# Performance work log

Measured on AMD Instinct MI355X. Metric: run time of the kernel, lower is better.

The kernel has to match this reference:

```python
import jax, jax.numpy as jnp
import numpy as np
from jax import lax

B, C, H, W, P = 16, 256, 64, 64, 4
EPS = 1e-5


def setup_inputs() -> dict:
    key = jax.random.key(0)
    ks = jax.random.split(key, 16)
    s = 0.05
    d = {
        'rgb': jax.random.normal(ks[0], (B, C, H, W), jnp.float32),
        'th': jax.random.normal(ks[1], (B, C, H, W), jnp.float32),
        'q_w': jax.random.normal(ks[2], (C, C), jnp.float32) * s,
        'q_b': jax.random.normal(ks[3], (C,), jnp.float32) * s,
        'kvr_w': jax.random.normal(ks[4], (2 * C, C), jnp.float32) * s,
        'kvr_b': jax.random.normal(ks[5], (2 * C,), jnp.float32) * s,
        'kvt_w': jax.random.normal(ks[6], (2 * C, C), jnp.float32) * s,
        'kvt_b': jax.random.normal(ks[7], (2 * C,), jnp.float32) * s,
        'offr_w': jax.random.normal(ks[8], (2 * P, C, 3, 3), jnp.float32) * s,
        'offr_b': jax.random.normal(ks[9], (2 * P,), jnp.float32) * s,
        'offt_w': jax.random.normal(ks[10], (2 * P, C, 3, 3), jnp.float32) * s,
        'offt_b': jax.random.normal(ks[11], (2 * P,), jnp.float32) * s,
        'out_w': jax.random.normal(ks[12], (C, 2 * C), jnp.float32) * s,
        'out_b': jax.random.normal(ks[13], (C,), jnp.float32) * s,
        'gamma': jnp.ones((C,), jnp.float32),
        'beta': jnp.zeros((C,), jnp.float32),
    }
    return d


def conv1x1(x, w, b):
    # x: [B,Ci,H,W], w: [Co,Ci] -> [B,Co,H,W]
    return jnp.einsum('bchw,oc->bohw', x, w) + b[None, :, None, None]


def conv3x3(x, w, b):
    y = lax.conv_general_dilated(x, w, (1, 1), 'SAME',
                                 dimension_numbers=('NCHW', 'OIHW', 'NCHW'))
    return y + b[None, :, None, None]


def deform_sample(feat, offset):
    # feat: [B,C,H,W]; offset: [B,2P,H,W] (pixel-unit offsets, (x,y) pairs)
    Bs, Cs, Hs, Ws = feat.shape
    off = offset.reshape(Bs, -1, 2, Hs, Ws)  # [B,P,2,H,W]
    # base grid in [-1,1], align_corners=True convention
    gy = jnp.linspace(-1.0, 1.0, Hs)[None, None, :, None]
    gx = jnp.linspace(-1.0, 1.0, Ws)[None, None, None, :]
    grid_x = gx + off[:, :, 0] / (Ws / 2.0)  # [B,P,H,W]
    grid_y = gy + off[:, :, 1] / (Hs / 2.0)
    # normalized -> pixel coords (align_corners=True)
    x = (grid_x + 1.0) * (Ws - 1) / 2.0
    y = (grid_y + 1.0) * (Hs - 1) / 2.0
    x0 = jnp.floor(x)
    y0 = jnp.floor(y)
    wx = x - x0
    wy = y - y0
    feat_flat = feat.reshape(Bs, Cs, Hs * Ws)

    def corner(xi, yi, wgt):
        valid = (xi >= 0) & (xi < Ws) & (yi >= 0) & (yi < Hs)  # zeros padding
        xc = jnp.clip(xi, 0, Ws - 1).astype(jnp.int32)
        yc = jnp.clip(yi, 0, Hs - 1).astype(jnp.int32)
        idx = (yc * Ws + xc).reshape(Bs, 1, -1)  # [B,1,P*H*W]
        g = jnp.take_along_axis(feat_flat, jnp.broadcast_to(idx, (Bs, Cs, idx.shape[-1])), axis=2)
        g = g.reshape(Bs, Cs, -1, Hs, Ws)  # [B,C,P,H,W]
        w_eff = (wgt * valid.astype(feat.dtype))[:, None]  # [B,1,P,H,W]
        return g * w_eff

    x0i = x0.astype(jnp.int32)
    y0i = y0.astype(jnp.int32)
    out = (corner(x0i, y0i, (1 - wx) * (1 - wy))
           + corner(x0i + 1, y0i, wx * (1 - wy))
           + corner(x0i, y0i + 1, (1 - wx) * wy)
           + corner(x0i + 1, y0i + 1, wx * wy))
    return out.mean(axis=2)  # mean over P -> [B,C,H,W]


def batchnorm_train(x, gamma, beta):
    mu = x.mean(axis=(0, 2, 3), keepdims=True)
    var = x.var(axis=(0, 2, 3), keepdims=True)
    xn = (x - mu) * lax.rsqrt(var + EPS)
    return xn * gamma[None, :, None, None] + beta[None, :, None, None]


def reference(rgb, th, q_w, q_b, kvr_w, kvr_b, kvt_w, kvt_b,
              offr_w, offr_b, offt_w, offt_b, out_w, out_b, gamma, beta):
    q_rgb = conv1x1(rgb, q_w, q_b)
    q_th = conv1x1(th, q_w, q_b)
    kv_rgb = conv1x1(rgb, kvr_w, kvr_b)
    kv_th = conv1x1(th, kvt_w, kvt_b)
    v_rgb = kv_rgb[:, C:]  # k_rgb = kv_rgb[:, :C] is unused downstream
    v_th = kv_th[:, C:]
    off_rgb2th = conv3x3(th, offr_w, offr_b)
    off_th2rgb = conv3x3(rgb, offt_w, offt_b)
    v_rgb2th = deform_sample(v_rgb, off_rgb2th)
    v_th2rgb = deform_sample(v_th, off_th2rgb)
    attn_rgb = jax.nn.sigmoid(q_rgb) * v_th2rgb
    attn_th = jax.nn.sigmoid(q_th) * v_rgb2th
    fused = conv1x1(jnp.concatenate([attn_rgb, attn_th], axis=1), out_w, out_b)
    return batchnorm_train(fused + 0.5 * (rgb + th), gamma, beta)
```

## Files before the change

kernel.cpp:

```cpp
#include <hip/hip_runtime.h>

typedef __bf16 bf16x8 __attribute__((ext_vector_type(8)));
typedef float  f32x4  __attribute__((ext_vector_type(4)));

constexpr int Bn = 16, Cn = 256, Hn = 64, Wn = 64, HWn = 64 * 64;
constexpr int Ntot = Bn * HWn;

#define DEV static __device__ __forceinline__

DEV unsigned short f2bf(float f) {
  unsigned u = __builtin_bit_cast(unsigned, f);
  u += 0x7fffu + ((u >> 16) & 1u);
  return (unsigned short)(u >> 16);
}
DEV float bf2f(unsigned short s) {
  unsigned u = ((unsigned)s) << 16;
  return __builtin_bit_cast(float, u);
}
DEV bf16x8 asbf(uint4 u) { return __builtin_bit_cast(bf16x8, u); }

__global__ void k_prep(const float* qw, const float* kvrw, const float* kvtw,
                       const float* offrw, const float* offtw, const float* outw,
                       unsigned short* Aqv, unsigned short* Aoff, unsigned short* Aout) {
  int idx = blockIdx.x * 256 + threadIdx.x;
  if (idx < 2 * 512 * 256) {
    int t = idx >> 17; int r = idx & 131071; int o = r >> 8; int c = r & 255;
    float v = (o < 256) ? qw[o * 256 + c] : (t ? kvtw[o * 256 + c] : kvrw[o * 256 + c]);
    Aqv[idx] = f2bf(v);
    return;
  }
  idx -= 2 * 512 * 256;
  if (idx < 2 * 16 * 2304) {
    int t = idx / 36864; int r = idx % 36864;
    int o = r / 2304; int rc = r % 2304; int tap = rc >> 8; int c = rc & 255;
    const float* w = t ? offtw : offrw;
    float v = (o < 8) ? w[(o * 256 + c) * 9 + tap] : 0.f;
    Aoff[idx] = f2bf(v);
    return;
  }
  idx -= 2 * 16 * 2304;
  if (idx < 256 * 512) Aout[idx] = f2bf(outw[idx]);
}

__global__ void k_transpose(const float* rgb, const float* th, unsigned short* xT) {
  int bi = blockIdx.x;
  int ct = bi & 3;
  int nt = (bi >> 2) & 63;
  int b  = (bi >> 8) & 15;
  int t  = bi >> 12;
  const float* src = t ? th : rgb;
  int c0 = ct * 64, n0 = nt * 64;
  __shared__ float tile[64][65];
  int tid = threadIdx.x;
  int nl = tid & 63, cg = tid >> 6;
#pragma unroll
  for (int i = 0; i < 16; i++) {
    int c = cg * 16 + i;
    tile[c][nl] = src[(size_t)(b * 256 + c0 + c) * HWn + n0 + nl];
  }
  __syncthreads();
  int pr = tid >> 2, sg = tid & 3;
  unsigned short tmp[16];
#pragma unroll
  for (int j = 0; j < 16; j++) tmp[j] = f2bf(tile[sg * 16 + j][pr]);
  unsigned short* dst = xT + (size_t)t * Ntot * 256 +
                        (size_t)(b * HWn + n0 + pr) * 256 + c0 + sg * 16;
  *(uint4*)(dst)     = *(const uint4*)(tmp);
  *(uint4*)(dst + 8) = *(const uint4*)(tmp + 8);
}

__global__ __launch_bounds__(512, 2) void k_qv(
    const unsigned short* Aqv, const unsigned short* xT,
    const float* qb, const float* kvrb, const float* kvtb,
    unsigned short* qs, unsigned short* vv) {
  __shared__ unsigned short smem[32768];
  int t  = blockIdx.z;
  int mt = blockIdx.y;
  int nt = blockIdx.x;
  int swznt = ((nt & 7) << 6) | (nt >> 3);
  int o0 = mt * 128;
  int n0 = swznt * 128;
  int tid = threadIdx.x;
  const unsigned short* Aq = Aqv + t * 512 * 256;
  const unsigned short* Xg = xT + (size_t)t * Ntot * 256 + (size_t)n0 * 256;

  auto stage = [&](int kb, int bb) {
    unsigned short* As = smem + bb * 8192;
    unsigned short* Xs = smem + 16384 + bb * 8192;
#pragma unroll
    for (int i = 0; i < 2; i++) {
      int cid = tid + i * 512;
      int row = cid >> 3, seg = cid & 7;
      int ss = seg ^ (row & 7);
      *(uint4*)(&As[row * 64 + seg * 8]) =
          *(const uint4*)(Aq + (size_t)(o0 + row) * 256 + kb * 64 + ss * 8);
    }
#pragma unroll
    for (int i = 0; i < 2; i++) {
      int cid = tid + i * 512;
      int row = cid >> 3, seg = cid & 7;
      int ss = seg ^ (row & 7);
      *(uint4*)(&Xs[row * 64 + seg * 8]) =
          *(const uint4*)(Xg + (size_t)row * 256 + kb * 64 + ss * 8);
    }
  };

  int w = __builtin_amdgcn_readfirstlane(tid >> 6);
  int lane = tid & 63;
  int wo = w & 1, wn = w >> 1;
  int r16 = lane & 15, q4 = lane >> 4;

  f32x4 acc[4][2];
#pragma unroll
  for (int a = 0; a < 4; a++) { acc[a][0] = f32x4{0.f,0.f,0.f,0.f}; acc[a][1] = f32x4{0.f,0.f,0.f,0.f}; }

  stage(0, 0);
  __syncthreads();
#pragma unroll
  for (int kb = 0; kb < 4; kb++) {
    if (kb < 3) stage(kb + 1, (kb + 1) & 1);
    const unsigned short* As = smem + (kb & 1) * 8192;
    const unsigned short* Xs = smem + 16384 + (kb & 1) * 8192;
#pragma unroll
    for (int ks = 0; ks < 2; ks++) {
      uint4 af[4], bfr[2];
#pragma unroll
      for (int oi = 0; oi < 4; oi++) {
        int row = wo * 64 + oi * 16 + r16;
        int seg = (ks * 4 + q4) ^ (row & 7);
        af[oi] = *(const uint4*)(&As[row * 64 + seg * 8]);
      }
#pragma unroll
      for (int ni = 0; ni < 2; ni++) {
        int row = wn * 32 + ni * 16 + r16;
        int seg = (ks * 4 + q4) ^ (row & 7);
        bfr[ni] = *(const uint4*)(&Xs[row * 64 + seg * 8]);
      }
#pragma unroll
      for (int oi = 0; oi < 4; oi++)
#pragma unroll
        for (int ni = 0; ni < 2; ni++)
          acc[oi][ni] = __builtin_amdgcn_mfma_f32_16x16x32_bf16(
              asbf(af[oi]), asbf(bfr[ni]), acc[oi][ni], 0, 0, 0);
    }
    __syncthreads();
  }

  bool isq = (mt < 2);
  const float* bias = isq ? qb : (t ? kvtb : kvrb);
  float4 bv[4];
#pragma unroll
  for (int oi = 0; oi < 4; oi++)
    bv[oi] = *(const float4*)(&bias[o0 + wo * 64 + oi * 16 + q4 * 4]);
#pragma unroll
  for (int oi = 0; oi < 4; oi++) {
    int ol = wo * 64 + oi * 16 + q4 * 4;
#pragma unroll
    for (int ni = 0; ni < 2; ni++) {
      int nl = wn * 32 + ni * 16 + r16;
      unsigned short pk[4];
#pragma unroll
      for (int j = 0; j < 4; j++) {
        float val = acc[oi][ni][j] + ((const float*)&bv[oi])[j];
        if (isq) val = 1.f / (1.f + __expf(-val));
        pk[j] = f2bf(val);
      }
      *(uint2*)(&smem[nl * 132 + ol]) = *(const uint2*)(pk);
    }
  }
  __syncthreads();
  unsigned short* outp = (isq ? qs : vv) + (size_t)t * Ntot * 256 + (mt & 1) * 128;
#pragma unroll
  for (int pass = 0; pass < 4; pass++) {
    int nl = pass * 32 + (tid >> 4);
    int c  = tid & 15;
    uint4 vq = *(const uint4*)(&smem[nl * 132 + c * 8]);
    *(uint4*)(outp + (size_t)(n0 + nl) * 256 + c * 8) = vq;
  }
}

__global__ __launch_bounds__(256, 4) void k_off(
    const unsigned short* Aoff, const unsigned short* xT,
    const float* offrb, const float* offtb, float* offo) {
  __shared__ unsigned short Alds[9 * 8 * 264 + 264];
  int t  = blockIdx.y;
  int bh = blockIdx.x;
  int swz = ((bh & 7) << 7) | (bh >> 3);
  int b = swz >> 6, h = swz & 63;
  int tid = threadIdx.x;
  const unsigned short* Aw = Aoff + t * 36864;

#pragma unroll
  for (int i = 0; i < 9; i++) {
    int cid = tid + i * 256;
    int o = cid / 288;
    int rem = cid - o * 288;
    int tap = rem >> 5, cg = rem & 31;
    uint4 v = *(const uint4*)(Aw + o * 2304 + tap * 256 + cg * 8);
    *(uint4*)(&Alds[(tap * 8 + o) * 264 + cg * 8]) = v;
  }
  if (tid < 33) {
    uint4 z; z.x = 0; z.y = 0; z.z = 0; z.w = 0;
    *(uint4*)(&Alds[19008 + tid * 8]) = z;
  }
  __syncthreads();

  int lane = tid & 63, w = tid >> 6;
  int r16 = lane & 15, q4 = lane >> 4;
  int wl = w * 16 + r16;
  const unsigned short* xin = xT + (size_t)(t ? 0 : 1) * Ntot * 256;
  int zbase = 19008 + q4 * 8;
  int abase = r16 * 264 + q4 * 8;
  bool rowok = (r16 < 8);

  f32x4 acc = {0.f, 0.f, 0.f, 0.f};
  uint4 bufA[8], bufB[8];

#define LOADT(buf, tap) {                                                      \
    int dy = (tap) / 3 - 1, dx = (tap) % 3 - 1;                                \
    int hh = h + dy, ww = wl + dx;                                             \
    bool ok = (hh >= 0 && hh < 64 && ww >= 0 && ww < 64);                      \
    int hc = hh < 0 ? 0 : (hh > 63 ? 63 : hh);                                 \
    int wc = ww < 0 ? 0 : (ww > 63 ? 63 : ww);                                 \
    const unsigned short* p =                                                  \
        xin + (size_t)(((b * 64 + hc) * 64 + wc) * 256) + q4 * 8;              \
    _Pragma("unroll") for (int ks = 0; ks < 8; ks++) {                         \
      uint4 v = *(const uint4*)(p + ks * 32);                                  \
      if (!ok) { v.x = 0; v.y = 0; v.z = 0; v.w = 0; }                         \
      buf[ks] = v;                                                             \
    } }

#define COMPT(buf, tap) {                                                      \
    _Pragma("unroll") for (int ks = 0; ks < 8; ks++) {                         \
      int aofs = rowok ? ((tap) * 8 * 264 + abase + ks * 32) : (zbase + ks * 32); \
      uint4 af = *(const uint4*)(&Alds[aofs]);                                 \
      acc = __builtin_amdgcn_mfma_f32_16x16x32_bf16(asbf(af), asbf(buf[ks]),   \
                                                    acc, 0, 0, 0);             \
    } }

  LOADT(bufA, 0)
  LOADT(bufB, 1)
  COMPT(bufA, 0)
  LOADT(bufA, 2)
  COMPT(bufB, 1)
  LOADT(bufB, 3)
  COMPT(bufA, 2)
  LOADT(bufA, 4)
  COMPT(bufB, 3)
  LOADT(bufB, 5)
  COMPT(bufA, 4)
  LOADT(bufA, 6)
  COMPT(bufB, 5)
  LOADT(bufB, 7)
  COMPT(bufA, 6)
  LOADT(bufA, 8)
  COMPT(bufB, 7)
  COMPT(bufA, 8)
#undef LOADT
#undef COMPT

  if (lane < 32) {
    const float* ob = t ? offtb : offrb;
    int n = (b * 64 + h) * 64 + wl;
    float4 r;
    r.x = acc[0] + ob[q4 * 4 + 0];
    r.y = acc[1] + ob[q4 * 4 + 1];
    r.z = acc[2] + ob[q4 * 4 + 2];
    r.w = acc[3] + ob[q4 * 4 + 3];
    *(float4*)(offo + (size_t)t * Ntot * 8 + (size_t)n * 8 + q4 * 4) = r;
  }
}

__global__ void k_gather(const unsigned short* qs, const unsigned short* vv,
                         const float* offo, unsigned short* concat) {
  int tid = threadIdx.x;
  int bi  = blockIdx.x;
  int pass = blockIdx.y;
  int swz = ((bi & 7) << 9) | (bi >> 3);
  int chunk = tid & 15, pixL = tid >> 4;
  int n = swz * 16 + pixL;
  int b = n >> 12;
  int h = (n >> 6) & 63, pix = n & 63;
  const unsigned short* vsrc = vv + (size_t)(pass ? 0 : 1) * Ntot * 256;
  const float* offp          = offo + (size_t)(pass ? 0 : 1) * Ntot * 8;
  const unsigned short* qsrc = qs + (size_t)(pass ? 1 : 0) * Ntot * 256;
  float acc[16];
#pragma unroll
  for (int i = 0; i < 16; i++) acc[i] = 0.f;
#pragma unroll
  for (int p = 0; p < 4; p++) {
    float dx = offp[(size_t)n * 8 + 2 * p], dy = offp[(size_t)n * 8 + 2 * p + 1];
    float xf = (float)pix + dx * (63.f / 64.f);
    float yf = (float)h   + dy * (63.f / 64.f);
    float x0f = floorf(xf), y0f = floorf(yf);
    float wx = xf - x0f, wy = yf - y0f;
    int x0 = (int)x0f, y0 = (int)y0f;
#pragma unroll
    for (int cc = 0; cc < 4; cc++) {
      int cy = cc >> 1, cx = cc & 1;
      int ix = x0 + cx, iy = y0 + cy;
      bool ok = (ix >= 0 && ix < 64 && iy >= 0 && iy < 64);
      int ixc = ix < 0 ? 0 : (ix > 63 ? 63 : ix);
      int iyc = iy < 0 ? 0 : (iy > 63 ? 63 : iy);
      float wgt = (cx ? wx : 1.f - wx) * (cy ? wy : 1.f - wy);
      wgt = ok ? wgt : 0.f;
      const unsigned short* g =
          vsrc + (size_t)(((b * 64 + iyc) * 64 + ixc) * 256 + chunk * 16);
      uint4 raw0 = *(const uint4*)(g);
      uint4 raw1 = *(const uint4*)(g + 8);
      const unsigned short* r0 = (const unsigned short*)&raw0;
      const unsigned short* r1 = (const unsigned short*)&raw1;
#pragma unroll
      for (int e = 0; e < 8; e++) {
        acc[e]     += wgt * bf2f(r0[e]);
        acc[8 + e] += wgt * bf2f(r1[e]);
      }
    }
  }
  uint4 q0 = *(const uint4*)(qsrc + (size_t)n * 256 + chunk * 16);
  uint4 q1 = *(const uint4*)(qsrc + (size_t)n * 256 + chunk * 16 + 8);
  const unsigned short* qp0 = (const unsigned short*)&q0;
  const unsigned short* qp1 = (const unsigned short*)&q1;
  unsigned short pk[16];
#pragma unroll
  for (int e = 0; e < 8; e++) {
    pk[e]     = f2bf(0.25f * acc[e]     * bf2f(qp0[e]));
    pk[8 + e] = f2bf(0.25f * acc[8 + e] * bf2f(qp1[e]));
  }
  unsigned short* dst = concat + (size_t)n * 512 + pass * 256 + chunk * 16;
  *(uint4*)(dst)     = *(const uint4*)(pk);
  *(uint4*)(dst + 8) = *(const uint4*)(pk + 8);
}

__global__ __launch_bounds__(512, 2) void k_out(
    const unsigned short* Aout, const unsigned short* concat, const float* outb,
    const float* rgb, const float* th, float* dout, float* partial) {
  __shared__ unsigned short Asm[2][128 * 64];
  __shared__ unsigned short Xsm[2][128 * 64];
  __shared__ float bstat[128][2];
  int bi = blockIdx.x;
  int my = blockIdx.y;
  int swz = ((bi & 7) << 6) | (bi >> 3);
  int n0 = swz * 128;
  int o0 = my * 128;
  int tid = threadIdx.x;
  if (tid < 128) { bstat[tid][0] = 0.f; bstat[tid][1] = 0.f; }

  auto stage = [&](int kb, int bb) {
#pragma unroll
    for (int i = 0; i < 2; i++) {
      int cid = tid + i * 512;
      int row = cid >> 3, seg = cid & 7;
      int ss = seg ^ (row & 7);
      *(uint4*)(&Asm[bb][row * 64 + seg * 8]) =
          *(const uint4*)(Aout + (size_t)(o0 + row) * 512 + kb * 64 + ss * 8);
    }
#pragma unroll
    for (int i = 0; i < 2; i++) {
      int cid = tid + i * 512;
      int row = cid >> 3, seg = cid & 7;
      int ss = seg ^ (row & 7);
      *(uint4*)(&Xsm[bb][row * 64 + seg * 8]) =
          *(const uint4*)(concat + (size_t)(n0 + row) * 512 + kb * 64 + ss * 8);
    }
  };

  int w = __builtin_amdgcn_readfirstlane(tid >> 6);
  int lane = tid & 63;
  int wo = w & 1, wn = w >> 1;
  int r16 = lane & 15, q4 = lane >> 4;

  f32x4 acc2[4][2];
#pragma unroll
  for (int a = 0; a < 4; a++) { acc2[a][0] = f32x4{0.f,0.f,0.f,0.f}; acc2[a][1] = f32x4{0.f,0.f,0.f,0.f}; }

  stage(0, 0);
  __syncthreads();
#pragma unroll
  for (int kb = 0; kb < 8; kb++) {
    if (kb < 7) stage(kb + 1, (kb + 1) & 1);
    int bb = kb & 1;
#pragma unroll
    for (int ks = 0; ks < 2; ks++) {
      uint4 af[4], bfr[2];
#pragma unroll
      for (int oi = 0; oi < 4; oi++) {
        int row = wo * 64 + oi * 16 + r16;
        int seg = (ks * 4 + q4) ^ (row & 7);
        af[oi] = *(const uint4*)(&Asm[bb][row * 64 + seg * 8]);
      }
#pragma unroll
      for (int ni = 0; ni < 2; ni++) {
        int row = wn * 32 + ni * 16 + r16;
        int seg = (ks * 4 + q4) ^ (row & 7);
        bfr[ni] = *(const uint4*)(&Xsm[bb][row * 64 + seg * 8]);
      }
#pragma unroll
      for (int oi = 0; oi < 4; oi++)
#pragma unroll
        for (int ni = 0; ni < 2; ni++)
          acc2[oi][ni] = __builtin_amdgcn_mfma_f32_16x16x32_bf16(
              asbf(af[oi]), asbf(bfr[ni]), acc2[oi][ni], 0, 0, 0);
    }
    __syncthreads();
  }
#pragma unroll
  for (int oi = 0; oi < 4; oi++) {
    int obl = wo * 64 + oi * 16 + q4 * 4;
#pragma unroll
    for (int j = 0; j < 4; j++) {
      int ol = obl + j;
      int o = o0 + ol;
      float s1 = 0.f, s2 = 0.f;
#pragma unroll
      for (int ni = 0; ni < 2; ni++) {
        int pl = wn * 32 + ni * 16 + r16;
        int n = n0 + pl;
        int bI = n >> 12, hw = n & 4095;
        size_t gidx = (size_t)(bI * 256 + o) * HWn + hw;
        float val = acc2[oi][ni][j] + outb[o] + 0.5f * (rgb[gidx] + th[gidx]);
        dout[gidx] = val;
        s1 += val; s2 += val * val;
      }
#pragma unroll
      for (int m = 1; m < 16; m <<= 1) {
        s1 += __shfl_xor(s1, m, 16);
        s2 += __shfl_xor(s2, m, 16);
      }
      if (r16 == 0) { atomicAdd(&bstat[ol][0], s1); atomicAdd(&bstat[ol][1], s2); }
    }
  }
  __syncthreads();
  if (tid < 128) {
    partial[((size_t)my * 512 + bi) * 256 + tid]       = bstat[tid][0];
    partial[((size_t)my * 512 + bi) * 256 + 128 + tid] = bstat[tid][1];
  }
}

__global__ void k_stats(const float* partial, const float* gamma, const float* beta,
                        float* sstats) {
  int c = blockIdx.x, tid = threadIdx.x;
  int my = c >> 7, j = c & 127;
  float s1 = 0.f, s2 = 0.f;
  for (int i = tid; i < 512; i += 256) {
    const float* pp = partial + ((size_t)my * 512 + i) * 256;
    s1 += pp[j];
    s2 += pp[128 + j];
  }
  __shared__ float r1[256], r2[256];
  r1[tid] = s1; r2[tid] = s2;
  __syncthreads();
  for (int st = 128; st > 0; st >>= 1) {
    if (tid < st) { r1[tid] += r1[tid + st]; r2[tid] += r2[tid + st]; }
    __syncthreads();
  }
  if (tid == 0) {
    float mean = r1[0] / 65536.f;
    float var  = r2[0] / 65536.f - mean * mean;
    float scale = gamma[c] / sqrtf(var + 1e-5f);
    sstats[c]       = scale;
    sstats[256 + c] = beta[c] - mean * scale;
  }
}

__global__ void k_bn(float* dout, const float* sstats) {
  int idx = blockIdx.x * 256 + threadIdx.x;
  size_t base = (size_t)idx * 4;
  int c = (int)((base >> 12) & 255);
  float4 v = *(float4*)(dout + base);
  float sc = sstats[c], sh = sstats[256 + c];
  v.x = v.x * sc + sh; v.y = v.y * sc + sh;
  v.z = v.z * sc + sh; v.w = v.w * sc + sh;
  *(float4*)(dout + base) = v;
}

extern "C" void kernel_launch(void* const* d_in, const int* in_sizes, int n_in,
                              void* d_out, int out_size, void* d_ws, size_t ws_size,
                              hipStream_t stream) {
  const float* rgb   = (const float*)d_in[0];
  const float* th    = (const float*)d_in[1];
  const float* qw    = (const float*)d_in[2];
  const float* qb    = (const float*)d_in[3];
  const float* kvrw  = (const float*)d_in[4];
  const float* kvrb  = (const float*)d_in[5];
  const float* kvtw  = (const float*)d_in[6];
  const float* kvtb  = (const float*)d_in[7];
  const float* offrw = (const float*)d_in[8];
  const float* offrb = (const float*)d_in[9];
  const float* offtw = (const float*)d_in[10];
  const float* offtb = (const float*)d_in[11];
  const float* outw  = (const float*)d_in[12];
  const float* outb  = (const float*)d_in[13];
  const float* gamma = (const float*)d_in[14];
  const float* beta  = (const float*)d_in[15];
  float* dout = (float*)d_out;

  unsigned short* xT   = (unsigned short*)d_ws;
  unsigned short* qsb  = xT  + (size_t)2 * Ntot * 256;
  unsigned short* vvb  = qsb + (size_t)2 * Ntot * 256;
  float* offo          = (float*)(vvb + (size_t)2 * Ntot * 256);
  unsigned short* Aqv  = (unsigned short*)(offo + (size_t)2 * Ntot * 8);
  unsigned short* Aoff = Aqv + 2 * 512 * 256;
  unsigned short* Aout = Aoff + 2 * 16 * 2304;
  float* partial       = (float*)(Aout + 256 * 512);
  float* sstats        = partial + (size_t)1024 * 256;
  unsigned short* concat = xT;

  k_prep<<<1824, 256, 0, stream>>>(qw, kvrw, kvtw, offrw, offtw, outw, Aqv, Aoff, Aout);
  k_transpose<<<8192, 256, 0, stream>>>(rgb, th, xT);
  k_qv<<<dim3(512, 4, 2), 512, 0, stream>>>(Aqv, xT, qb, kvrb, kvtb, qsb, vvb);
  k_off<<<dim3(1024, 2), 256, 0, stream>>>(Aoff, xT, offrb, offtb, offo);
  k_gather<<<dim3(4096, 2), 256, 0, stream>>>(qsb, vvb, offo, concat);
  k_out<<<dim3(512, 2), 512, 0, stream>>>(Aout, concat, outb, rgb, th, dout, partial);
  k_stats<<<256, 256, 0, stream>>>(partial, gamma, beta, sstats);
  k_bn<<<16384, 256, 0, stream>>>(dout, sstats);
}
```

Before: 406.2 us.

## Fuse deformable gather into output projection GEMM via shared-memory concat tile

Merges the gather kernel and the output 1x1 conv GEMM into one kernel. Each block handles one image row of 64 pixels: it bilinearly samples and gates both streams into a 64x512 bf16 tile in LDS, then runs the 256-output MFMA GEMM straight from LDS with weight fragments read from global memory in a repacked layout. This removes the global concat write and reread and one launch. In exchange it uses 64 KB of LDS per block, loses the double-buffered staging of the weights, and doubles the number of BN partial rows.

Result: slower. 567.8 us (+39.8%).

```diff
diff --git a/kernel.cpp b/kernel.cpp
--- a/kernel.cpp
+++ b/kernel.cpp
@@ -39,7 +39,10 @@
     return;
   }
   idx -= 2 * 16 * 2304;
-  if (idx < 256 * 512) Aout[idx] = f2bf(outw[idx]);
+  if (idx < 256 * 512) {
+    int seg = idx >> 11, o = (idx >> 3) & 255, e = idx & 7;
+    Aout[idx] = f2bf(outw[o * 512 + seg * 8 + e]);
+  }
 }
 
 __global__ void k_transpose(const float* rgb, const float* th, unsigned short* xT) {
@@ -271,153 +274,122 @@
   }
 }
 
-__global__ void k_gather(const unsigned short* qs, const unsigned short* vv,
-                         const float* offo, unsigned short* concat) {
+__global__ __launch_bounds__(512, 2) void k_fuse(
+    const unsigned short* qs, const unsigned short* vv, const float* offo,
+    const unsigned short* Apk, const float* outb,
+    const float* rgb, const float* th, float* dout, float* partial) {
+  __shared__ unsigned short cc[64 * 512];
+  __shared__ float bstat[256][2];
   int tid = threadIdx.x;
   int bi  = blockIdx.x;
-  int pass = blockIdx.y;
-  int swz = ((bi & 7) << 9) | (bi >> 3);
-  int chunk = tid & 15, pixL = tid >> 4;
-  int n = swz * 16 + pixL;
-  int b = n >> 12;
-  int h = (n >> 6) & 63, pix = n & 63;
-  const unsigned short* vsrc = vv + (size_t)(pass ? 0 : 1) * Ntot * 256;
-  const float* offp          = offo + (size_t)(pass ? 0 : 1) * Ntot * 8;
-  const unsigned short* qsrc = qs + (size_t)(pass ? 1 : 0) * Ntot * 256;
-  float acc[16];
-#pragma unroll
-  for (int i = 0; i < 16; i++) acc[i] = 0.f;
-#pragma unroll
-  for (int p = 0; p < 4; p++) {
-    float dx = offp[(size_t)n * 8 + 2 * p], dy = offp[(size_t)n * 8 + 2 * p + 1];
-    float xf = (float)pix + dx * (63.f / 64.f);
-    float yf = (float)h   + dy * (63.f / 64.f);
-    float x0f = floorf(xf), y0f = floorf(yf);
-    float wx = xf - x0f, wy = yf - y0f;
-    int x0 = (int)x0f, y0 = (int)y0f;
-#pragma unroll
-    for (int cc = 0; cc < 4; cc++) {
-      int cy = cc >> 1, cx = cc & 1;
-      int ix = x0 + cx, iy = y0 + cy;
-      bool ok = (ix >= 0 && ix < 64 && iy >= 0 && iy < 64);
-      int ixc = ix < 0 ? 0 : (ix > 63 ? 63 : ix);
-      int iyc = iy < 0 ? 0 : (iy > 63 ? 63 : iy);
-      float wgt = (cx ? wx : 1.f - wx) * (cy ? wy : 1.f - wy);
-      wgt = ok ? wgt : 0.f;
-      const unsigned short* g =
-          vsrc + (size_t)(((b * 64 + iyc) * 64 + ixc) * 256 + chunk * 16);
-      uint4 raw0 = *(const uint4*)(g);
-      uint4 raw1 = *(const uint4*)(g + 8);
-      const unsigned short* r0 = (const unsigned short*)&raw0;
-      const unsigned short* r1 = (const unsigned short*)&raw1;
+  int swz = ((bi & 7) << 7) | (bi >> 3);
+  int b = swz >> 6, h = swz & 63;
+  if (tid < 256) { bstat[tid][0] = 0.f; bstat[tid][1] = 0.f; }
+
+  {
+    int px = tid >> 3, sub = tid & 7;
+    int pass = sub >> 2, qtr = sub & 3;
+    int n = (b * 64 + h) * 64 + px;
+    const unsigned short* vsrc = vv + (size_t)(pass ? 0 : 1) * Ntot * 256;
+    const float* offp          = offo + (size_t)(pass ? 0 : 1) * Ntot * 8 + (size_t)n * 8;
+    const unsigned short* qsrc = qs + (size_t)(pass ? 1 : 0) * Ntot * 256 + (size_t)n * 256;
+
+    int   coff[4][4];
+    float cwgt[4][4];
+#pragma unroll
+    for (int p = 0; p < 4; p++) {
+      float dx = offp[2 * p], dy = offp[2 * p + 1];
+      float xf = (float)px + dx * (63.f / 64.f);
+      float yf = (float)h  + dy * (63.f / 64.f);
+      float x0f = floorf(xf), y0f = floorf(yf);
+      float wx = xf - x0f, wy = yf - y0f;
+      int x0 = (int)x0f, y0 = (int)y0f;
+#pragma unroll
+      for (int c = 0; c < 4; c++) {
+        int cy2 = c >> 1, cx2 = c & 1;
+        int ix = x0 + cx2, iy = y0 + cy2;
+        bool ok = (ix >= 0 && ix < 64 && iy >= 0 && iy < 64);
+        int ixc = ix < 0 ? 0 : (ix > 63 ? 63 : ix);
+        int iyc = iy < 0 ? 0 : (iy > 63 ? 63 : iy);
+        coff[p][c] = ((b * 64 + iyc) * 64 + ixc) * 256;
+        float wgt = (cx2 ? wx : 1.f - wx) * (cy2 ? wy : 1.f - wy);
+        cwgt[p][c] = ok ? wgt : 0.f;
+      }
+    }
+#pragma unroll
+    for (int s = 0; s < 4; s++) {
+      int c0 = qtr * 64 + s * 16;
+      float acc[16];
+#pragma unroll
+      for (int i = 0; i < 16; i++) acc[i] = 0.f;
+#pragma unroll
+      for (int p = 0; p < 4; p++)
+#pragma unroll
+        for (int c = 0; c < 4; c++) {
+          const unsigned short* g = vsrc + coff[p][c] + c0;
+          float wgt = cwgt[p][c];
+          uint4 raw0 = *(const uint4*)(g);
+          uint4 raw1 = *(const uint4*)(g + 8);
+          const unsigned short* r0 = (const unsigned short*)&raw0;
+          const unsigned short* r1 = (const unsigned short*)&raw1;
+#pragma unroll
+          for (int e = 0; e < 8; e++) {
+            acc[e]     += wgt * bf2f(r0[e]);
+            acc[8 + e] += wgt * bf2f(r1[e]);
+          }
+        }
+      uint4 q0 = *(const uint4*)(qsrc + c0);
+      uint4 q1 = *(const uint4*)(qsrc + c0 + 8);
+      const unsigned short* qp0 = (const unsigned short*)&q0;
+      const unsigned short* qp1 = (const unsigned short*)&q1;
+      unsigned short pk[16];
 #pragma unroll
       for (int e = 0; e < 8; e++) {
-        acc[e]     += wgt * bf2f(r0[e]);
-        acc[8 + e] += wgt * bf2f(r1[e]);
-      }
-    }
-  }
-  uint4 q0 = *(const uint4*)(qsrc + (size_t)n * 256 + chunk * 16);
-  uint4 q1 = *(const uint4*)(qsrc + (size_t)n * 256 + chunk * 16 + 8);
-  const unsigned short* qp0 = (const unsigned short*)&q0;
-  const unsigned short* qp1 = (const unsigned short*)&q1;
-  unsigned short pk[16];
-#pragma unroll
-  for (int e = 0; e < 8; e++) {
-    pk[e]     = f2bf(0.25f * acc[e]     * bf2f(qp0[e]));
-    pk[8 + e] = f2bf(0.25f * acc[8 + e] * bf2f(qp1[e]));
-  }
-  unsigned short* dst = concat + (size_t)n * 512 + pass * 256 + chunk * 16;
-  *(uint4*)(dst)     = *(const uint4*)(pk);
-  *(uint4*)(dst + 8) = *(const uint4*)(pk + 8);
-}
-
-__global__ __launch_bounds__(512, 2) void k_out(
-    const unsigned short* Aout, const unsigned short* concat, const float* outb,
-    const float* rgb, const float* th, float* dout, float* partial) {
-  __shared__ unsigned short Asm[2][128 * 64];
-  __shared__ unsigned short Xsm[2][128 * 64];
-  __shared__ float bstat[128][2];
-  int bi = blockIdx.x;
-  int my = blockIdx.y;
-  int swz = ((bi & 7) << 6) | (bi >> 3);
-  int n0 = swz * 128;
-  int o0 = my * 128;
-  int tid = threadIdx.x;
-  if (tid < 128) { bstat[tid][0] = 0.f; bstat[tid][1] = 0.f; }
-
-  auto stage = [&](int kb, int bb) {
-#pragma unroll
-    for (int i = 0; i < 2; i++) {
-      int cid = tid + i * 512;
-      int row = cid >> 3, seg = cid & 7;
-      int ss = seg ^ (row & 7);
-      *(uint4*)(&Asm[bb][row * 64 + seg * 8]) =
-          *(const uint4*)(Aout + (size_t)(o0 + row) * 512 + kb * 64 + ss * 8);
-    }
-#pragma unroll
-    for (int i = 0; i < 2; i++) {
-      int cid = tid + i * 512;
-      int row = cid >> 3, seg = cid & 7;
-      int ss = seg ^ (row & 7);
-      *(uint4*)(&Xsm[bb][row * 64 + seg * 8]) =
-          *(const uint4*)(concat + (size_t)(n0 + row) * 512 + kb * 64 + ss * 8);
-    }
-  };
-
-  int w = __builtin_amdgcn_readfirstlane(tid >> 6);
-  int lane = tid & 63;
-  int wo = w & 1, wn = w >> 1;
+        pk[e]     = f2bf(0.25f * acc[e]     * bf2f(qp0[e]));
+        pk[8 + e] = f2bf(0.25f * acc[8 + e] * bf2f(qp1[e]));
+      }
+      int seg0 = pass * 32 + qtr * 8 + s * 2;
+      *(uint4*)(&cc[px * 512 + ((seg0    ) ^ (px & 7)) * 8]) = *(const uint4*)(pk);
+      *(uint4*)(&cc[px * 512 + ((seg0 + 1) ^ (px & 7)) * 8]) = *(const uint4*)(pk + 8);
+    }
+  }
+  __syncthreads();
+
+  int lane = tid & 63, wv = tid >> 6;
+  int wo = wv >> 1, wn = wv & 1;
   int r16 = lane & 15, q4 = lane >> 4;
-
   f32x4 acc2[4][2];
 #pragma unroll
   for (int a = 0; a < 4; a++) { acc2[a][0] = f32x4{0.f,0.f,0.f,0.f}; acc2[a][1] = f32x4{0.f,0.f,0.f,0.f}; }
-
-  stage(0, 0);
-  __syncthreads();
-#pragma unroll
-  for (int kb = 0; kb < 8; kb++) {
-    if (kb < 7) stage(kb + 1, (kb + 1) & 1);
-    int bb = kb & 1;
-#pragma unroll
-    for (int ks = 0; ks < 2; ks++) {
-      uint4 af[4], bfr[2];
-#pragma unroll
-      for (int oi = 0; oi < 4; oi++) {
-        int row = wo * 64 + oi * 16 + r16;
-        int seg = (ks * 4 + q4) ^ (row & 7);
-        af[oi] = *(const uint4*)(&Asm[bb][row * 64 + seg * 8]);
-      }
-#pragma unroll
-      for (int ni = 0; ni < 2; ni++) {
-        int row = wn * 32 + ni * 16 + r16;
-        int seg = (ks * 4 + q4) ^ (row & 7);
-        bfr[ni] = *(const uint4*)(&Xsm[bb][row * 64 + seg * 8]);
-      }
-#pragma unroll
-      for (int oi = 0; oi < 4; oi++)
-#pragma unroll
-        for (int ni = 0; ni < 2; ni++)
-          acc2[oi][ni] = __builtin_amdgcn_mfma_f32_16x16x32_bf16(
-              asbf(af[oi]), asbf(bfr[ni]), acc2[oi][ni], 0, 0, 0);
-    }
-    __syncthreads();
+#pragma unroll
+  for (int kst = 0; kst < 16; kst++) {
+    uint4 bfr[2];
+#pragma unroll
+    for (int ni = 0; ni < 2; ni++) {
+      int row = wn * 32 + ni * 16 + r16;
+      int slot = (kst * 4 + q4) ^ (row & 7);
+      bfr[ni] = *(const uint4*)(&cc[row * 512 + slot * 8]);
+    }
+#pragma unroll
+    for (int oi = 0; oi < 4; oi++) {
+      int o = wo * 64 + oi * 16 + r16;
+      uint4 a = *(const uint4*)(Apk + (size_t)((kst * 4 + q4) * 256 + o) * 8);
+      acc2[oi][0] = __builtin_amdgcn_mfma_f32_16x16x32_bf16(asbf(a), asbf(bfr[0]), acc2[oi][0], 0, 0, 0);
+      acc2[oi][1] = __builtin_amdgcn_mfma_f32_16x16x32_bf16(asbf(a), asbf(bfr[1]), acc2[oi][1], 0, 0, 0);
+    }
   }
 #pragma unroll
   for (int oi = 0; oi < 4; oi++) {
-    int obl = wo * 64 + oi * 16 + q4 * 4;
+    int ob = wo * 64 + oi * 16 + q4 * 4;
 #pragma unroll
     for (int j = 0; j < 4; j++) {
-      int ol = obl + j;
-      int o = o0 + ol;
+      int o = ob + j;
       float s1 = 0.f, s2 = 0.f;
 #pragma unroll
       for (int ni = 0; ni < 2; ni++) {
         int pl = wn * 32 + ni * 16 + r16;
-        int n = n0 + pl;
-        int bI = n >> 12, hw = n & 4095;
-        size_t gidx = (size_t)(bI * 256 + o) * HWn + hw;
+        int hw = h * 64 + pl;
+        size_t gidx = (size_t)(b * 256 + o) * HWn + hw;
         float val = acc2[oi][ni][j] + outb[o] + 0.5f * (rgb[gidx] + th[gidx]);
         dout[gidx] = val;
         s1 += val; s2 += val * val;
@@ -427,25 +399,23 @@
         s1 += __shfl_xor(s1, m, 16);
         s2 += __shfl_xor(s2, m, 16);
       }
-      if (r16 == 0) { atomicAdd(&bstat[ol][0], s1); atomicAdd(&bstat[ol][1], s2); }
-    }
-  }
-  __syncthreads();
-  if (tid < 128) {
-    partial[((size_t)my * 512 + bi) * 256 + tid]       = bstat[tid][0];
-    partial[((size_t)my * 512 + bi) * 256 + 128 + tid] = bstat[tid][1];
+      if (r16 == 0) { atomicAdd(&bstat[o][0], s1); atomicAdd(&bstat[o][1], s2); }
+    }
+  }
+  __syncthreads();
+  if (tid < 256) {
+    partial[(size_t)bi * 512 + tid]       = bstat[tid][0];
+    partial[(size_t)bi * 512 + 256 + tid] = bstat[tid][1];
   }
 }
 
 __global__ void k_stats(const float* partial, const float* gamma, const float* beta,
                         float* sstats) {
   int c = blockIdx.x, tid = threadIdx.x;
-  int my = c >> 7, j = c & 127;
   float s1 = 0.f, s2 = 0.f;
-  for (int i = tid; i < 512; i += 256) {
-    const float* pp = partial + ((size_t)my * 512 + i) * 256;
-    s1 += pp[j];
-    s2 += pp[128 + j];
+  for (int i = tid; i < 1024; i += 256) {
+    s1 += partial[(size_t)i * 512 + c];
+    s2 += partial[(size_t)i * 512 + 256 + c];
   }
   __shared__ float r1[256], r2[256];
   r1[tid] = s1; r2[tid] = s2;
@@ -503,15 +473,13 @@
   unsigned short* Aoff = Aqv + 2 * 512 * 256;
   unsigned short* Aout = Aoff + 2 * 16 * 2304;
   float* partial       = (float*)(Aout + 256 * 512);
-  float* sstats        = partial + (size_t)1024 * 256;
-  unsigned short* concat = xT;
+  float* sstats        = partial + (size_t)1024 * 512;
 
   k_prep<<<1824, 256, 0, stream>>>(qw, kvrw, kvtw, offrw, offtw, outw, Aqv, Aoff, Aout);
   k_transpose<<<8192, 256, 0, stream>>>(rgb, th, xT);
   k_qv<<<dim3(512, 4, 2), 512, 0, stream>>>(Aqv, xT, qb, kvrb, kvtb, qsb, vvb);
   k_off<<<dim3(1024, 2), 256, 0, stream>>>(Aoff, xT, offrb, offtb, offo);
-  k_gather<<<dim3(4096, 2), 256, 0, stream>>>(qsb, vvb, offo, concat);
-  k_out<<<dim3(512, 2), 512, 0, stream>>>(Aout, concat, outb, rgb, th, dout, partial);
+  k_fuse<<<1024, 512, 0, stream>>>(qsb, vvb, offo, Aout, outb, rgb, th, dout, partial);
   k_stats<<<256, 256, 0, stream>>>(partial, gamma, beta, sstats);
   k_bn<<<16384, 256, 0, stream>>>(dout, sstats);
 }
```
